# Performance work log

Measured on AMD Instinct MI355X. Metric: run time of the kernel, lower is better.

## Reference

```python
import jax, jax.numpy as jnp
import numpy as np

B, S, HID = 2, 2048, 2048
H, KV, D = 16, 4, 128
THETA = 10000.0


def _apply_rope(x):
    # x: [B, h, S, D]; rotate even/odd interleaved halves, concat (original layout)
    seq = x.shape[2]
    pos = jnp.arange(seq, dtype=jnp.float32)
    inv_freq = 1.0 / (THETA ** (jnp.arange(0, D, 2, dtype=jnp.float32) / D))
    freqs = pos[:, None] * inv_freq[None, :]            # [S, D/2]
    cos = jnp.cos(freqs)[None, None]                    # [1,1,S,D/2]
    sin = jnp.sin(freqs)[None, None]
    x1, x2 = x[..., ::2], x[..., 1::2]
    return jnp.concatenate([x1 * cos - x2 * sin, x1 * sin + x2 * cos], axis=-1)


def setup_inputs() -> dict:
    key = jax.random.key(0)
    ks = jax.random.split(key, 5)
    x = jax.random.normal(ks[0], (B, S, HID), jnp.float32)
    Wq = jax.random.normal(ks[1], (HID, H * D), jnp.float32) * 0.02
    Wk = jax.random.normal(ks[2], (HID, KV * D), jnp.float32) * 0.02
    Wv = jax.random.normal(ks[3], (HID, KV * D), jnp.float32) * 0.02
    Wo = jax.random.normal(ks[4], (H * D, HID), jnp.float32) * 0.02
    mask = jnp.tril(jnp.ones((S, S), jnp.int32))[None, None]  # causal [1,1,S,S]
    return {"x": x, "mask": mask, "Wq": Wq, "Wk": Wk, "Wv": Wv, "Wo": Wo}


def reference(x, mask, Wq, Wk, Wv, Wo):
    b, s, _ = x.shape
    q = (x @ Wq).reshape(b, s, H, D).transpose(0, 2, 1, 3)   # [B,H,S,D]
    k = (x @ Wk).reshape(b, s, KV, D).transpose(0, 2, 1, 3)  # [B,KV,S,D]
    v = (x @ Wv).reshape(b, s, KV, D).transpose(0, 2, 1, 3)
    q = _apply_rope(q)
    k = _apply_rope(k)
    rep = H // KV
    k = jnp.repeat(k, rep, axis=1)  # GQA repeat_interleave -> [B,H,S,D]
    v = jnp.repeat(v, rep, axis=1)
    scores = jnp.einsum('bhqd,bhkd->bhqk', q, k) / jnp.sqrt(jnp.float32(D))
    scores = jnp.where(mask == 0, -jnp.inf, scores)
    attn = jax.nn.softmax(scores, axis=-1)  # dropout p=0 -> identity
    out = jnp.einsum('bhqk,bhkd->bhqd', attn, v)
    out = out.transpose(0, 2, 1, 3).reshape(b, s, H * D)
    return out @ Wo
```

## Files before the change

kernel.cpp:

```cpp
#include <hip/hip_runtime.h>
#include <cstdint>


typedef __attribute__((ext_vector_type(8))) short short8;
typedef __attribute__((ext_vector_type(4))) float f32x4;
typedef __attribute__((ext_vector_type(16))) float f32x16;
typedef unsigned short u16;
typedef unsigned int u32;

#define NLOG_THETA_D2 (-0.14391156831212787f)
#define QSC_L2E 0.12751779437543f
#define M2SHIFT 17.3123404906676f

__device__ __forceinline__ u16 f2bf(float f) {
    u32 u = __float_as_uint(f);
    u += 0x7fffu + ((u >> 16) & 1u);
    return (u16)(u >> 16);
}
__device__ __forceinline__ float bf2f(u16 u) { return __uint_as_float(((u32)u) << 16); }
__device__ __forceinline__ float fast_exp2(float x) { return __builtin_amdgcn_exp2f(x); }

__device__ __forceinline__ void async_copy16(const void* g, void* lds) {
    __builtin_amdgcn_global_load_lds(
        (const __attribute__((address_space(1))) u32*)(uintptr_t)g,
        (__attribute__((address_space(3))) u32*)(uintptr_t)lds, 16, 0, 0);
}

__global__ __launch_bounds__(256)
void prep_kernel(const float* __restrict__ x, const float* __restrict__ Wq,
                 const float* __restrict__ Wk, const float* __restrict__ Wv,
                 u16* __restrict__ xb, u16* __restrict__ Wqkvt) {
    __shared__ float tile[32][33];
    int blk = blockIdx.x;
    if (blk < 8192) {
        int i = blk * 256 + threadIdx.x;
        float4 v = ((const float4*)x)[i];
        ushort4 o;
        o.x = f2bf(v.x); o.y = f2bf(v.y); o.z = f2bf(v.z); o.w = f2bf(v.w);
        ((ushort4*)xb)[i] = o;
        return;
    }
    const float* in; int C, orow, bx, by;
    if (blk < 12288)      { int j = blk - 8192;  in = Wq; C = 2048; orow = 0;    bx = j & 63; by = j >> 6; }
    else if (blk < 13312) { int j = blk - 12288; in = Wk; C = 512;  orow = 2048; bx = j & 15; by = j >> 4; }
    else                  { int j = blk - 13312; in = Wv; C = 512;  orow = 2560; bx = j & 15; by = j >> 4; }
    int r0 = by * 32, c0 = bx * 32;
    int tx = threadIdx.x & 31, ty = threadIdx.x >> 5;
#pragma unroll
    for (int j = 0; j < 4; ++j)
        tile[ty + j * 8][tx] = in[(size_t)(r0 + ty + j * 8) * C + c0 + tx];
    __syncthreads();
#pragma unroll
    for (int j = 0; j < 4; ++j)
        Wqkvt[(size_t)(orow + c0 + ty + j * 8) * 2048 + r0 + tx] = f2bf(tile[tx][ty + j * 8]);
}

__global__ __launch_bounds__(256)
void rope_vt_kernel(const u16* __restrict__ qkv, const float* __restrict__ Wo,
                    u16* __restrict__ qR, u16* __restrict__ kR,
                    u16* __restrict__ vT, u16* __restrict__ Wot) {
    int blk = blockIdx.x;
    if (blk < 4096) {
        int row = blk;
        float pos = (float)(row & 2047);
        const u16* rbase = qkv + (size_t)row * 3072;
        for (int t = threadIdx.x; t < 640; t += 256) {
            ushort4 uv; int c4; u16* ob; float sc;
            if (t < 512) {
                c4 = t * 4; uv = *(const ushort4*)(rbase + c4);
                ob = qR + (size_t)row * 2048 + (c4 & ~127); sc = QSC_L2E;
            } else {
                int u = t - 512; c4 = u * 4; uv = *(const ushort4*)(rbase + 2048 + c4);
                ob = kR + (size_t)row * 512 + (c4 & ~127); sc = 1.0f;
            }
            int j = (c4 & 127) >> 1;
            float x0 = bf2f(uv.x), x1 = bf2f(uv.y), x2 = bf2f(uv.z), x3 = bf2f(uv.w);
            float s1, c1, s2, c2;
            sincosf(pos * __expf(NLOG_THETA_D2 * (float)j), &s1, &c1);
            sincosf(pos * __expf(NLOG_THETA_D2 * (float)(j + 1)), &s2, &c2);
            float o1 = (x0 * c1 - x1 * s1) * sc;
            float o2 = (x2 * c2 - x3 * s2) * sc;
            float o3 = (x0 * s1 + x1 * c1) * sc;
            float o4 = (x2 * s2 + x3 * c2) * sc;
            *(u32*)&ob[j]      = (u32)f2bf(o1) | ((u32)f2bf(o2) << 16);
            *(u32*)&ob[64 + j] = (u32)f2bf(o3) | ((u32)f2bf(o4) << 16);
        }
        return;
    }
    int tx = threadIdx.x & 31, ty = threadIdx.x >> 5;
    if (blk < 6144) {
        __shared__ u16 tile[32][33];
        int j = blk - 4096;
        int b = j >> 10, rem = j & 1023;
        int c0 = (rem & 15) * 32, r0 = (rem >> 4) * 32;
        const u16* in = qkv + (size_t)b * 2048 * 3072 + 2560;
        u16* out = vT + (size_t)b * 512 * 2048;
#pragma unroll
        for (int i = 0; i < 4; ++i)
            tile[ty + i * 8][tx] = in[(size_t)(r0 + ty + i * 8) * 3072 + c0 + tx];
        __syncthreads();
#pragma unroll
        for (int i = 0; i < 4; ++i)
            out[(size_t)(c0 + ty + i * 8) * 2048 + r0 + tx] = tile[tx][ty + i * 8];
        return;
    }
    {
        __shared__ float tile[32][33];
        int j = blk - 6144;
        int c0 = (j & 63) * 32, r0 = (j >> 6) * 32;
#pragma unroll
        for (int i = 0; i < 4; ++i)
            tile[ty + i * 8][tx] = Wo[(size_t)(r0 + ty + i * 8) * 2048 + c0 + tx];
        __syncthreads();
#pragma unroll
        for (int i = 0; i < 4; ++i)
            Wot[(size_t)(c0 + ty + i * 8) * 2048 + r0 + tx] = f2bf(tile[tx][ty + i * 8]);
    }
}

template <int OBF>
__global__ __launch_bounds__(256)
void gemm_bf16(const u16* __restrict__ A, const u16* __restrict__ Bt,
               void* __restrict__ Cout, int M, int N, int K) {
    __shared__ __align__(16) u16 As[128 * 32];
    __shared__ __align__(16) u16 Bs[128 * 32];
    const int tid = threadIdx.x, wid = tid >> 6, lane = tid & 63;
    const int quad = lane >> 4, l16 = lane & 15;
    const int m0 = blockIdx.y * 128, n0 = blockIdx.x * 128;
    const int wm0 = (wid >> 1) * 64, wn0 = (wid & 1) * 64;
    f32x4 acc[4][4] = {};

    for (int k0 = 0; k0 < K; k0 += 32) {
#pragma unroll
        for (int rr = 0; rr < 2; ++rr) {
            int s = rr * 256 + wid * 64 + lane;
            int row = s >> 2;
            int c = (s & 3) ^ ((row >> 1) & 3);
            async_copy16(A + (size_t)(m0 + row) * K + k0 + c * 8,
                         &As[(size_t)(rr * 256 + wid * 64) * 8]);
            async_copy16(Bt + (size_t)(n0 + row) * K + k0 + c * 8,
                         &Bs[(size_t)(rr * 256 + wid * 64) * 8]);
        }
        __syncthreads();
        short8 a[4], b[4];
#pragma unroll
        for (int i = 0; i < 4; ++i) {
            int ra = wm0 + i * 16 + l16;
            a[i] = *(const short8*)&As[ra * 32 + ((quad ^ ((ra >> 1) & 3)) << 3)];
            int rb = wn0 + i * 16 + l16;
            b[i] = *(const short8*)&Bs[rb * 32 + ((quad ^ ((rb >> 1) & 3)) << 3)];
        }
#pragma unroll
        for (int i = 0; i < 4; ++i)
#pragma unroll
            for (int j = 0; j < 4; ++j)
                acc[i][j] = __builtin_amdgcn_mfma_f32_16x16x32_bf16(a[i], b[j], acc[i][j], 0, 0, 0);
        __syncthreads();
    }
#pragma unroll
    for (int i = 0; i < 4; ++i) {
        int rb = m0 + wm0 + i * 16 + quad * 4;
#pragma unroll
        for (int j = 0; j < 4; ++j) {
            int col = n0 + wn0 + j * 16 + l16;
#pragma unroll
            for (int r = 0; r < 4; ++r) {
                if (OBF) ((u16*)Cout)[(size_t)(rb + r) * N + col] = f2bf(acc[i][j][r]);
                else     ((float*)Cout)[(size_t)(rb + r) * N + col] = acc[i][j][r];
            }
        }
    }
}

__global__ __launch_bounds__(256, 2)
void attn_kernel(const u16* __restrict__ qR, const u16* __restrict__ kR,
                 const u16* __restrict__ vT, u16* __restrict__ ao) {
    __shared__ __align__(16) u16 bufK[64 * 128];
    __shared__ __align__(16) u16 bufV[128 * 64];
    const int tid = threadIdx.x, wid = tid >> 6, lane = tid & 63;
    const int l31 = lane & 31, h = lane >> 5;
    const int b = blockIdx.z, hh = blockIdx.y;
    const int qt = b ? blockIdx.x : (15 - blockIdx.x);
    const int kvh = hh >> 2;
    const int q0 = qt * 128;
    const u16* kB = kR + (size_t)b * 2048 * 512 + kvh * 128;
    const u16* vB = vT + (size_t)(b * 512 + kvh * 128) * 2048;

    const int rq = wid * 32 + l31;
    const u16* qrow = qR + (size_t)(b * 2048 + q0 + rq) * 2048 + hh * 128;
    short8 aQ[8];
#pragma unroll
    for (int kd = 0; kd < 8; ++kd)
        aQ[kd] = *(const short8*)(qrow + kd * 16 + h * 8);

    f32x16 oacc[4] = {};
    float lp = 0.f;
    const int qg = q0 + rq;
    const int ntiles = 2 * qt + 2;

    for (int t = 0; t < ntiles; ++t) {
        const int kk0 = t * 64;
#pragma unroll
        for (int rr = 0; rr < 4; ++rr) {
            int s = rr * 256 + wid * 64 + lane;
            int rK = s >> 4, cK = (s & 15) ^ (rK & 7);
            async_copy16(kB + (size_t)(kk0 + rK) * 512 + cK * 8,
                         &bufK[(size_t)(rr * 256 + wid * 64) * 8]);
            int rV = s >> 3, cV = (s & 7) ^ (rV & 7);
            async_copy16(vB + (size_t)rV * 2048 + kk0 + cV * 8,
                         &bufV[(size_t)(rr * 256 + wid * 64) * 8]);
        }
        __syncthreads();

        f32x16 sacc[2] = {};
#pragma unroll
        for (int kd = 0; kd < 8; ++kd)
#pragma unroll
            for (int mt = 0; mt < 2; ++mt) {
                int rk = mt * 32 + l31;
                short8 aK = *(const short8*)&bufK[rk * 128 + (((kd * 2 + h) ^ (rk & 7)) << 3)];
                sacc[mt] = __builtin_amdgcn_mfma_f32_32x32x16_bf16(aK, aQ[kd], sacc[mt], 0, 0, 0);
            }

        u32 pk[2][8];
        const bool domask = (t >= ntiles - 2);
        auto softpack = [&](bool dm) {
#pragma unroll
            for (int mt = 0; mt < 2; ++mt) {
                const int kvb = kk0 + mt * 32 + 4 * h;
#pragma unroll
                for (int p = 0; p < 8; ++p) {
                    int r0 = 2 * p;
                    float s0 = sacc[mt][r0], s1 = sacc[mt][r0 + 1];
                    float p0, p1;
                    if (dm) {
                        int kv0 = kvb + (r0 & 3) + 8 * (r0 >> 2);
                        p0 = (kv0 <= qg)     ? fast_exp2(s0 - M2SHIFT) : 0.f;
                        p1 = (kv0 + 1 <= qg) ? fast_exp2(s1 - M2SHIFT) : 0.f;
                    } else {
                        p0 = fast_exp2(s0 - M2SHIFT);
                        p1 = fast_exp2(s1 - M2SHIFT);
                    }
                    lp += p0 + p1;
                    pk[mt][p] = (u32)f2bf(p0) | ((u32)f2bf(p1) << 16);
                }
            }
        };
        if (domask) softpack(true); else softpack(false);

#pragma unroll
        for (int ks = 0; ks < 4; ++ks) {
            int mt = ks >> 1, k2 = ks & 1;
            u32 own0 = pk[mt][4 * k2 + 2 * h + 0];
            u32 own1 = pk[mt][4 * k2 + 2 * h + 1];
            u32 snd0 = pk[mt][4 * k2 + 2 * (h ^ 1) + 0];
            u32 snd1 = pk[mt][4 * k2 + 2 * (h ^ 1) + 1];
            u32 rc0 = __shfl_xor((int)snd0, 32, 64);
            u32 rc1 = __shfl_xor((int)snd1, 32, 64);
            union { short8 v; u32 u[4]; } bP;
            bP.u[0] = h ? rc0 : own0;
            bP.u[1] = h ? rc1 : own1;
            bP.u[2] = h ? own0 : rc0;
            bP.u[3] = h ? own1 : rc1;
#pragma unroll
            for (int dt = 0; dt < 4; ++dt) {
                int rv = dt * 32 + l31;
                short8 aV = *(const short8*)&bufV[rv * 64 + (((ks * 2 + h) ^ (rv & 7)) << 3)];
                oacc[dt] = __builtin_amdgcn_mfma_f32_32x32x16_bf16(aV, bP.v, oacc[dt], 0, 0, 0);
            }
        }
        __syncthreads();
    }

    lp += __shfl_xor(lp, 32, 64);
    float linv = 1.0f / lp;
    u16* orow = ao + (size_t)(b * 2048 + qg) * 2048 + hh * 128;
#pragma unroll
    for (int dt = 0; dt < 4; ++dt)
#pragma unroll
        for (int g = 0; g < 4; ++g) {
            ushort4 o4;
            o4.x = f2bf(oacc[dt][4 * g + 0] * linv);
            o4.y = f2bf(oacc[dt][4 * g + 1] * linv);
            o4.z = f2bf(oacc[dt][4 * g + 2] * linv);
            o4.w = f2bf(oacc[dt][4 * g + 3] * linv);
            *(ushort4*)&orow[dt * 32 + 8 * g + 4 * h] = o4;
        }
}

extern "C" void kernel_launch(void* const* d_in, const int* in_sizes, int n_in,
                              void* d_out, int out_size, void* d_ws, size_t ws_size,
                              hipStream_t stream) {
    const float* x  = (const float*)d_in[0];
    const float* Wq = (const float*)d_in[2];
    const float* Wk = (const float*)d_in[3];
    const float* Wv = (const float*)d_in[4];
    const float* Wo = (const float*)d_in[5];
    float* out = (float*)d_out;

    char* ws = (char*)d_ws;
    u16* Wqkvt = (u16*)(ws);
    u16* Wot   = Wqkvt;
    u16* xb_ao = (u16*)(ws + 12582912);
    u16* qkv   = (u16*)(ws + 29360128);
    u16* qR    = (u16*)(ws + 54525952);
    u16* kR    = (u16*)(ws + 71303168);
    u16* vT    = (u16*)(ws + 75497472);

    dim3 blk(256);
    prep_kernel<<<14336, blk, 0, stream>>>(x, Wq, Wk, Wv, xb_ao, Wqkvt);
    gemm_bf16<1><<<dim3(24, 32), blk, 0, stream>>>(xb_ao, Wqkvt, qkv, 4096, 3072, 2048);
    rope_vt_kernel<<<10240, blk, 0, stream>>>(qkv, Wo, qR, kR, vT, Wot);
    attn_kernel<<<dim3(16, 16, 2), blk, 0, stream>>>(qR, kR, vT, xb_ao);
    gemm_bf16<0><<<dim3(16, 32), blk, 0, stream>>>(xb_ao, Wot, out, 4096, 2048, 2048);
}
```

Baseline: 368.4 us.

## Double-buffer K/V tiles in attention and switch PV matmul to fp16

Attention now holds two LDS buffers for K and V and issues the async copy of the next tile before computing on the current one, so global loads overlap the QK and PV MFMAs. This removes one barrier per iteration and doubles LDS use, which may limit occupancy. Separately, V is stored as fp16 during the transpose prep, and probabilities are packed with the hardware cvt_pkrtz instead of manual bf16 rounding. The PV product then uses the f16 MFMA, which cuts ALU work in softmax packing but changes precision, and fp16 range could matter for large V values.

```diff
diff --git a/kernel.cpp b/kernel.cpp
--- a/kernel.cpp
+++ b/kernel.cpp
@@ -3,6 +3,8 @@
 
 
 typedef __attribute__((ext_vector_type(8))) short short8;
+typedef __attribute__((ext_vector_type(8))) _Float16 half8;
+typedef __attribute__((ext_vector_type(2))) __fp16 fp16x2;
 typedef __attribute__((ext_vector_type(4))) float f32x4;
 typedef __attribute__((ext_vector_type(16))) float f32x16;
 typedef unsigned short u16;
@@ -18,6 +20,11 @@
     return (u16)(u >> 16);
 }
 __device__ __forceinline__ float bf2f(u16 u) { return __uint_as_float(((u32)u) << 16); }
+__device__ __forceinline__ u16 bf2h(u16 b) {
+    union { _Float16 h; u16 u; } cv;
+    cv.h = (_Float16)bf2f(b);
+    return cv.u;
+}
 __device__ __forceinline__ float fast_exp2(float x) { return __builtin_amdgcn_exp2f(x); }
 
 __device__ __forceinline__ void async_copy16(const void* g, void* lds) {
@@ -101,7 +108,7 @@
         __syncthreads();
 #pragma unroll
         for (int i = 0; i < 4; ++i)
-            out[(size_t)(c0 + ty + i * 8) * 2048 + r0 + tx] = tile[tx][ty + i * 8];
+            out[(size_t)(c0 + ty + i * 8) * 2048 + r0 + tx] = bf2h(tile[tx][ty + i * 8]);
         return;
     }
     {
@@ -175,8 +182,8 @@
 __global__ __launch_bounds__(256, 2)
 void attn_kernel(const u16* __restrict__ qR, const u16* __restrict__ kR,
                  const u16* __restrict__ vT, u16* __restrict__ ao) {
-    __shared__ __align__(16) u16 bufK[64 * 128];
-    __shared__ __align__(16) u16 bufV[128 * 64];
+    __shared__ __align__(16) u16 bufK[2][64 * 128];
+    __shared__ __align__(16) u16 bufV[2][128 * 64];
     const int tid = threadIdx.x, wid = tid >> 6, lane = tid & 63;
     const int l31 = lane & 31, h = lane >> 5;
     const int b = blockIdx.z, hh = blockIdx.y;
@@ -186,6 +193,26 @@
     const u16* kB = kR + (size_t)b * 2048 * 512 + kvh * 128;
     const u16* vB = vT + (size_t)(b * 512 + kvh * 128) * 2048;
 
+    const u16* kSrc[4]; const u16* vSrc[4]; int ldsOff[4];
+#pragma unroll
+    for (int rr = 0; rr < 4; ++rr) {
+        int s = rr * 256 + wid * 64 + lane;
+        int rK = s >> 4, cK = (s & 15) ^ (rK & 7);
+        kSrc[rr] = kB + (size_t)rK * 512 + cK * 8;
+        int rV = s >> 3, cV = (s & 7) ^ (rV & 7);
+        vSrc[rr] = vB + (size_t)rV * 2048 + cV * 8;
+        ldsOff[rr] = (rr * 256 + wid * 64) * 8;
+    }
+    auto stage = [&](int buf) {
+#pragma unroll
+        for (int rr = 0; rr < 4; ++rr) {
+            async_copy16(kSrc[rr], &bufK[buf][ldsOff[rr]]);
+            async_copy16(vSrc[rr], &bufV[buf][ldsOff[rr]]);
+            kSrc[rr] += 64 * 512;
+            vSrc[rr] += 64;
+        }
+    };
+
     const int rq = wid * 32 + l31;
     const u16* qrow = qR + (size_t)(b * 2048 + q0 + rq) * 2048 + hh * 128;
     short8 aQ[8];
@@ -198,19 +225,11 @@
     const int qg = q0 + rq;
     const int ntiles = 2 * qt + 2;
 
+    stage(0);
     for (int t = 0; t < ntiles; ++t) {
-        const int kk0 = t * 64;
-#pragma unroll
-        for (int rr = 0; rr < 4; ++rr) {
-            int s = rr * 256 + wid * 64 + lane;
-            int rK = s >> 4, cK = (s & 15) ^ (rK & 7);
-            async_copy16(kB + (size_t)(kk0 + rK) * 512 + cK * 8,
-                         &bufK[(size_t)(rr * 256 + wid * 64) * 8]);
-            int rV = s >> 3, cV = (s & 7) ^ (rV & 7);
-            async_copy16(vB + (size_t)rV * 2048 + kk0 + cV * 8,
-                         &bufV[(size_t)(rr * 256 + wid * 64) * 8]);
-        }
-        __syncthreads();
+        const int cur = t & 1;
+        __syncthreads();
+        if (t + 1 < ntiles) stage(cur ^ 1);
 
         f32x16 sacc[2] = {};
 #pragma unroll
@@ -218,10 +237,11 @@
 #pragma unroll
             for (int mt = 0; mt < 2; ++mt) {
                 int rk = mt * 32 + l31;
-                short8 aK = *(const short8*)&bufK[rk * 128 + (((kd * 2 + h) ^ (rk & 7)) << 3)];
+                short8 aK = *(const short8*)&bufK[cur][rk * 128 + (((kd * 2 + h) ^ (rk & 7)) << 3)];
                 sacc[mt] = __builtin_amdgcn_mfma_f32_32x32x16_bf16(aK, aQ[kd], sacc[mt], 0, 0, 0);
             }
 
+        const int kk0 = t * 64;
         u32 pk[2][8];
         const bool domask = (t >= ntiles - 2);
         auto softpack = [&](bool dm) {
@@ -242,7 +262,9 @@
                         p1 = fast_exp2(s1 - M2SHIFT);
                     }
                     lp += p0 + p1;
-                    pk[mt][p] = (u32)f2bf(p0) | ((u32)f2bf(p1) << 16);
+                    union { fp16x2 h; u32 u; } cv;
+                    cv.h = __builtin_amdgcn_cvt_pkrtz(p0, p1);
+                    pk[mt][p] = cv.u;
                 }
             }
         };
@@ -257,7 +279,7 @@
             u32 snd1 = pk[mt][4 * k2 + 2 * (h ^ 1) + 1];
             u32 rc0 = __shfl_xor((int)snd0, 32, 64);
             u32 rc1 = __shfl_xor((int)snd1, 32, 64);
-            union { short8 v; u32 u[4]; } bP;
+            union { half8 v; u32 u[4]; } bP;
             bP.u[0] = h ? rc0 : own0;
             bP.u[1] = h ? rc1 : own1;
             bP.u[2] = h ? own0 : rc0;
@@ -265,11 +287,11 @@
 #pragma unroll
             for (int dt = 0; dt < 4; ++dt) {
                 int rv = dt * 32 + l31;
-                short8 aV = *(const short8*)&bufV[rv * 64 + (((ks * 2 + h) ^ (rv & 7)) << 3)];
-                oacc[dt] = __builtin_amdgcn_mfma_f32_32x32x16_bf16(aV, bP.v, oacc[dt], 0, 0, 0);
-            }
-        }
-        __syncthreads();
+                union { short8 s; half8 v; } aV;
+                aV.s = *(const short8*)&bufV[cur][rv * 64 + (((ks * 2 + h) ^ (rv & 7)) << 3)];
+                oacc[dt] = __builtin_amdgcn_mfma_f32_32x32x16_f16(aV.v, bP.v, oacc[dt], 0, 0, 0);
+            }
+        }
     }
 
     lp += __shfl_xor(lp, 32, 64);
```

New measurement: 354.2 us. 3.9% less time.
